# Kernel optimization log

Hardware: AMD Instinct MI355X
Metric: run time of the kernel (lower is better)

The kernel has to match this reference:

```python
import jax, jax.numpy as jnp
import numpy as np

NUM_LABELS = 80
GROUPS = 512
OUT_PER_GROUP = 4  # 2048 / 512
K = 14  # kernel == spatial size -> 1x1 output


def setup_inputs() -> dict:
    key = jax.random.key(0)
    ks = jax.random.split(key, 8)
    B = 256
    x = jax.random.normal(ks[0], (B, NUM_LABELS, K, K), dtype=jnp.float32)
    # conv1: 1x1, num_labels -> 512 (store as [out,in])
    w1 = jax.random.normal(ks[1], (512, NUM_LABELS), dtype=jnp.float32) * 0.05
    b1 = jax.random.normal(ks[2], (512,), dtype=jnp.float32) * 0.01
    # conv2: 1x1, 512 -> 512
    w2 = jax.random.normal(ks[3], (512, 512), dtype=jnp.float32) * 0.05
    b2 = jax.random.normal(ks[4], (512,), dtype=jnp.float32) * 0.01
    # conv3 (grouped): per group, 1 in-ch -> 4 out-ch, 14x14 kernel, no bias
    w3 = jax.random.normal(ks[5], (GROUPS, OUT_PER_GROUP, K, K), dtype=jnp.float32) * 0.02
    # fc: 2048 -> num_labels (torch Linear layout [out,in])
    fc_w = jax.random.normal(ks[6], (NUM_LABELS, GROUPS * OUT_PER_GROUP), dtype=jnp.float32) * 0.02
    fc_b = jax.random.normal(ks[7], (NUM_LABELS,), dtype=jnp.float32) * 0.01
    return {"x": x, "w1": w1, "b1": b1, "w2": w2, "b2": b2,
            "w3": w3, "fc_w": fc_w, "fc_b": fc_b}


def reference(x, w1, b1, w2, b2, w3, fc_w, fc_b):
    # conv1: 1x1 conv == channel GEMM. x: [B,C,H,W]
    h = jnp.einsum('bchw,oc->bohw', x, w1) + b1[None, :, None, None]
    # conv2: 1x1 conv, 512 -> 512
    h = jnp.einsum('bchw,oc->bohw', h, w2) + b2[None, :, None, None]
    # conv3: 512 independent group convs (1 in-ch each, full 14x14 kernel,
    # no padding) -> output spatial 1x1. Fused into a single contraction.
    # h: [B, G, H, W], w3: [G, O, H, W] -> [B, G, O]
    g = jnp.einsum('bghw,gohw->bgo', h, w3)
    g = jax.nn.relu(g)
    # torch.cat over groups then flatten == reshape [B, G*O]
    flat = g.reshape(g.shape[0], GROUPS * OUT_PER_GROUP)
    return flat @ fc_w.T + fc_b
```

## Files before the change

### kernel.cpp

```cpp
#include <hip/hip_runtime.h>
#include <hip/hip_bf16.h>

#define CIN 80
#define NSP 196
#define HWP 208
#define KP  96
#define XST 104

#define NBA 4096
#define NBB 1024
#define NBC 512
#define NBD 64
#define NBE 16

typedef __attribute__((ext_vector_type(8))) short  short8;
typedef __attribute__((ext_vector_type(4))) float  floatx4;
typedef __attribute__((ext_vector_type(4))) unsigned short ushort4v;

static __device__ __forceinline__ unsigned short f2b(float f) {
    __hip_bfloat16 h = __float2bfloat16(f);
    return *(unsigned short*)&h;
}
static __device__ __forceinline__ float b2f(unsigned short u) {
    unsigned int x = ((unsigned int)u) << 16;
    float f; __builtin_memcpy(&f, &x, 4); return f;
}

__global__ __launch_bounds__(384) void kPre(
    const float* __restrict__ x,  const float* __restrict__ w1,
    const float* __restrict__ b1, const float* __restrict__ w2,
    const float* __restrict__ b2, const float* __restrict__ w3,
    const float* __restrict__ fc_w, const float* __restrict__ fc_b,
    float* __restrict__ Wcf, unsigned short* __restrict__ xbf,
    unsigned short* __restrict__ w3tb, unsigned short* __restrict__ fctb,
    float* __restrict__ out)
{
    __shared__ float tile[80 * 53];
    const int blk = blockIdx.x, t = threadIdx.x;

    if (blk < NBA) {
        const int o4 = blk >> 5, kc = blk & 31;
        const int lc = t % 96, oi = t / 96;
        const int o = o4 * 4 + oi;
        const int m0 = kc * 16;
        if (lc <= CIN) {
            const float* __restrict__ w2p = w2 + (size_t)o * 512 + m0;
            float part = 0.f;
            if (lc < CIN) {
                const float* __restrict__ w1p = w1 + (size_t)m0 * CIN + lc;
                #pragma unroll
                for (int i = 0; i < 16; ++i)
                    part = fmaf(w2p[i], w1p[(size_t)i * CIN], part);
            } else {
                #pragma unroll
                for (int i = 0; i < 16; ++i)
                    part = fmaf(w2p[i], b1[m0 + i], part);
                if (kc == 31) part += b2[o];
            }
            atomicAdd(Wcf + o * KP + lc, part);
        }
    } else if (blk < NBA + NBB) {
        const int r = blk - NBA;
        const int b = r >> 2, qt = r & 3, hw0 = qt * 52;
        for (int idx = t; idx < 80 * 52; idx += 384) {
            const int k = idx / 52, hl = idx - k * 52;
            const int hw = hw0 + hl;
            tile[k * 53 + hl] = (hw < NSP) ? x[(size_t)b * CIN * NSP + k * NSP + hw] : 0.f;
        }
        __syncthreads();
        unsigned short* __restrict__ ob = xbf + (size_t)b * HWP * KP;
        for (int idx = t; idx < 52 * 24; idx += 384) {
            const int hl = idx / 24, kq = idx - hl * 24;
            const int hw = hw0 + hl;
            ushort4v v;
            #pragma unroll
            for (int j = 0; j < 4; ++j) {
                const int k = kq * 4 + j;
                float f = 0.f;
                if (hw < NSP) {
                    if (k < CIN) f = tile[k * 53 + hl];
                    else if (k == CIN) f = 1.f;
                }
                v[j] = f2b(f);
            }
            *(ushort4v*)(ob + (size_t)hw * KP + kq * 4) = v;
        }
    } else if (blk < NBA + NBB + NBC) {
        const int g = blk - NBA - NBB;
        if (t < HWP) {
            ushort4v v;
            #pragma unroll
            for (int o = 0; o < 4; ++o)
                v[o] = f2b((t < NSP) ? w3[(size_t)g * 4 * NSP + o * NSP + t] : 0.f);
            *(ushort4v*)(w3tb + ((size_t)g * HWP + t) * 4) = v;
        }
    } else if (blk < NBA + NBB + NBC + NBD) {
        const int base = (blk - NBA - NBB - NBC) * 2560;
        for (int i = t; i < 2560; i += 384) {
            const int idx = base + i;
            const int k = idx / CIN, l = idx - k * CIN;
            fctb[idx] = f2b(fc_w[(size_t)l * 2048 + k]);
        }
    } else {
        const int base = (blk - NBA - NBB - NBC - NBD) * 1280;
        for (int i = t; i < 1280; i += 384) {
            const int idx = base + i;
            out[idx] = fc_b[idx - (idx / CIN) * CIN];
        }
    }
}

__global__ __launch_bounds__(512) void kM(
    const unsigned short* __restrict__ xbf, const float* __restrict__ Wcf,
    const unsigned short* __restrict__ w3tb, const unsigned short* __restrict__ fctb,
    float* __restrict__ out)
{
    __shared__ __align__(16) unsigned short xs[HWP * XST];
    __shared__ float gl[1024];
    const int b = blockIdx.x, gc = blockIdx.y;
    const int t = threadIdx.x;

    {
        const ushort4v* __restrict__ src = (const ushort4v*)(xbf + (size_t)b * HWP * KP);
        for (int idx = t; idx < HWP * 24; idx += 512) {
            const int r = idx / 24, c = idx - r * 24;
            *(ushort4v*)(xs + r * XST + c * 4) = src[idx];
        }
    }

    const int w = t >> 6, lane = t & 63;
    const int col = lane & 15, quad = lane >> 4;
    const int gb = gc * 256 + w * 32;

    short8 A[2][3];
    #pragma unroll
    for (int mt = 0; mt < 2; ++mt) {
        const float* __restrict__ ap = Wcf + (size_t)(gb + mt * 16 + col) * KP + quad * 8;
        #pragma unroll
        for (int ks = 0; ks < 3; ++ks) {
            const floatx4 lo = *(const floatx4*)(ap + ks * 32);
            const floatx4 hi = *(const floatx4*)(ap + ks * 32 + 4);
            short8 s;
            #pragma unroll
            for (int j = 0; j < 4; ++j) {
                s[j]     = (short)f2b(lo[j]);
                s[4 + j] = (short)f2b(hi[j]);
            }
            A[mt][ks] = s;
        }
    }

    float p[2][4][4];
    #pragma unroll
    for (int mt = 0; mt < 2; ++mt)
        #pragma unroll
        for (int r = 0; r < 4; ++r)
            #pragma unroll
            for (int o = 0; o < 4; ++o) p[mt][r][o] = 0.f;

    const unsigned short* __restrict__ xrow = xs + col * XST + quad * 8;
    const unsigned short* __restrict__ wb0 =
        w3tb + ((size_t)(gb + quad * 4) * HWP + col) * 4;
    const unsigned short* __restrict__ wb1 =
        w3tb + ((size_t)(gb + 16 + quad * 4) * HWP + col) * 4;

    __syncthreads();

    #pragma unroll 1
    for (int nt = 0; nt < 13; ++nt) {
        ushort4v wv0[4], wv1[4];
        #pragma unroll
        for (int r = 0; r < 4; ++r) {
            wv0[r] = *(const ushort4v*)(wb0 + ((size_t)r * HWP + nt * 16) * 4);
            wv1[r] = *(const ushort4v*)(wb1 + ((size_t)r * HWP + nt * 16) * 4);
        }
        const unsigned short* __restrict__ xp = xrow + nt * 16 * XST;
        const short8 x0 = *(const short8*)(xp);
        const short8 x1 = *(const short8*)(xp + 32);
        const short8 x2 = *(const short8*)(xp + 64);
        floatx4 a0 = {0.f, 0.f, 0.f, 0.f}, a1 = {0.f, 0.f, 0.f, 0.f};
        a0 = __builtin_amdgcn_mfma_f32_16x16x32_bf16(A[0][0], x0, a0, 0, 0, 0);
        a0 = __builtin_amdgcn_mfma_f32_16x16x32_bf16(A[0][1], x1, a0, 0, 0, 0);
        a0 = __builtin_amdgcn_mfma_f32_16x16x32_bf16(A[0][2], x2, a0, 0, 0, 0);
        a1 = __builtin_amdgcn_mfma_f32_16x16x32_bf16(A[1][0], x0, a1, 0, 0, 0);
        a1 = __builtin_amdgcn_mfma_f32_16x16x32_bf16(A[1][1], x1, a1, 0, 0, 0);
        a1 = __builtin_amdgcn_mfma_f32_16x16x32_bf16(A[1][2], x2, a1, 0, 0, 0);
        #pragma unroll
        for (int r = 0; r < 4; ++r) {
            p[0][r][0] = fmaf(a0[r], b2f(wv0[r][0]), p[0][r][0]);
            p[0][r][1] = fmaf(a0[r], b2f(wv0[r][1]), p[0][r][1]);
            p[0][r][2] = fmaf(a0[r], b2f(wv0[r][2]), p[0][r][2]);
            p[0][r][3] = fmaf(a0[r], b2f(wv0[r][3]), p[0][r][3]);
            p[1][r][0] = fmaf(a1[r], b2f(wv1[r][0]), p[1][r][0]);
            p[1][r][1] = fmaf(a1[r], b2f(wv1[r][1]), p[1][r][1]);
            p[1][r][2] = fmaf(a1[r], b2f(wv1[r][2]), p[1][r][2]);
            p[1][r][3] = fmaf(a1[r], b2f(wv1[r][3]), p[1][r][3]);
        }
    }

    #pragma unroll
    for (int mt = 0; mt < 2; ++mt)
        #pragma unroll
        for (int r = 0; r < 4; ++r) {
            float q0 = p[mt][r][0], q1 = p[mt][r][1], q2 = p[mt][r][2], q3 = p[mt][r][3];
            #pragma unroll
            for (int s = 8; s >= 1; s >>= 1) {
                q0 += __shfl_down(q0, s, 16);
                q1 += __shfl_down(q1, s, 16);
                q2 += __shfl_down(q2, s, 16);
                q3 += __shfl_down(q3, s, 16);
            }
            if (col == 0) {
                const int glocal = w * 32 + mt * 16 + quad * 4 + r;
                floatx4 ov = {fmaxf(q0, 0.f), fmaxf(q1, 0.f), fmaxf(q2, 0.f), fmaxf(q3, 0.f)};
                *(floatx4*)(gl + glocal * 4) = ov;
            }
        }
    __syncthreads();

    if (t < 320) {
        const int l = t % CIN, q = t / CIN;
        const unsigned short* __restrict__ fr =
            fctb + (size_t)(gc * 1024 + q * 256) * CIN + l;
        const float* __restrict__ gp = gl + q * 256;
        float s = 0.f;
        #pragma unroll 4
        for (int kk = 0; kk < 256; ++kk)
            s = fmaf(gp[kk], b2f(fr[(size_t)kk * CIN]), s);
        atomicAdd(out + b * CIN + l, s);
    }
}

extern "C" void kernel_launch(void* const* d_in, const int* in_sizes, int n_in,
                              void* d_out, int out_size, void* d_ws, size_t ws_size,
                              hipStream_t stream) {
    const float* x    = (const float*)d_in[0];
    const float* w1   = (const float*)d_in[1];
    const float* b1   = (const float*)d_in[2];
    const float* w2   = (const float*)d_in[3];
    const float* b2   = (const float*)d_in[4];
    const float* w3   = (const float*)d_in[5];
    const float* fc_w = (const float*)d_in[6];
    const float* fc_b = (const float*)d_in[7];
    float* out = (float*)d_out;

    const int B = in_sizes[0] / (CIN * NSP);

    char* ws = (char*)d_ws;
    unsigned short* xbf = (unsigned short*)ws;
    size_t off = (size_t)B * HWP * KP * 2;
    float* Wcf = (float*)(ws + off);                   off += 512 * KP * 4;
    unsigned short* w3tb = (unsigned short*)(ws + off); off += (size_t)512 * HWP * 4 * 2;
    unsigned short* fctb = (unsigned short*)(ws + off);

    hipMemsetAsync(Wcf, 0, 512 * KP * 4, stream);
    kPre<<<NBA + NBB + NBC + NBD + NBE, 384, 0, stream>>>(
        x, w1, b1, w2, b2, w3, fc_w, fc_b, Wcf, xbf, w3tb, fctb, out);
    kM<<<dim3(B, 2), 512, 0, stream>>>(xbf, Wcf, w3tb, fctb, out);
}
```

Measured before the change: 138.3 us.

## Fuse x bf16 transpose into main kernel and replace atomics with split-K reduction

Removes the separate x transposition/bf16 staging pass by having the main kernel read fp32 x directly, convert it and transpose it into shared memory. The folded W2·W1 weight is now built as 8 partial slices plus a small reduction kernel that emits bf16, replacing the memset and float atomics. The main kernel now runs one 1024-thread block per batch covering all groups, and reduces the FC output in shared memory with the bias added, so the output atomics and the bias-init blocks are gone. The trade-offs are an extra kernel launch, strided transposing writes to shared memory, and half as many blocks in the main kernel.

```diff
diff --git a/kernel.cpp b/kernel.cpp
--- a/kernel.cpp
+++ b/kernel.cpp
@@ -7,11 +7,9 @@
 #define KP  96
 #define XST 104
 
-#define NBA 4096
-#define NBB 1024
+#define NBA 1024
 #define NBC 512
 #define NBD 64
-#define NBE 16
 
 typedef __attribute__((ext_vector_type(8))) short  short8;
 typedef __attribute__((ext_vector_type(4))) float  floatx4;
@@ -27,66 +25,35 @@
 }
 
 __global__ __launch_bounds__(384) void kPre(
-    const float* __restrict__ x,  const float* __restrict__ w1,
-    const float* __restrict__ b1, const float* __restrict__ w2,
-    const float* __restrict__ b2, const float* __restrict__ w3,
-    const float* __restrict__ fc_w, const float* __restrict__ fc_b,
-    float* __restrict__ Wcf, unsigned short* __restrict__ xbf,
-    unsigned short* __restrict__ w3tb, unsigned short* __restrict__ fctb,
-    float* __restrict__ out)
+    const float* __restrict__ w1, const float* __restrict__ b1,
+    const float* __restrict__ w2, const float* __restrict__ w3,
+    const float* __restrict__ fc_w,
+    float* __restrict__ Wcf8, unsigned short* __restrict__ w3tb,
+    unsigned short* __restrict__ fctb)
 {
-    __shared__ float tile[80 * 53];
     const int blk = blockIdx.x, t = threadIdx.x;
 
     if (blk < NBA) {
-        const int o4 = blk >> 5, kc = blk & 31;
-        const int lc = t % 96, oi = t / 96;
-        const int o = o4 * 4 + oi;
-        const int m0 = kc * 16;
-        if (lc <= CIN) {
+        const int o4 = blk >> 3, kc = blk & 7, m0 = kc * 64;
+        if (t < 324) {
+            const int lc = t % 81, oi = t / 81;
+            const int o = o4 * 4 + oi;
             const float* __restrict__ w2p = w2 + (size_t)o * 512 + m0;
             float part = 0.f;
             if (lc < CIN) {
                 const float* __restrict__ w1p = w1 + (size_t)m0 * CIN + lc;
-                #pragma unroll
-                for (int i = 0; i < 16; ++i)
+                #pragma unroll 8
+                for (int i = 0; i < 64; ++i)
                     part = fmaf(w2p[i], w1p[(size_t)i * CIN], part);
             } else {
-                #pragma unroll
-                for (int i = 0; i < 16; ++i)
+                #pragma unroll 8
+                for (int i = 0; i < 64; ++i)
                     part = fmaf(w2p[i], b1[m0 + i], part);
-                if (kc == 31) part += b2[o];
             }
-            atomicAdd(Wcf + o * KP + lc, part);
-        }
-    } else if (blk < NBA + NBB) {
-        const int r = blk - NBA;
-        const int b = r >> 2, qt = r & 3, hw0 = qt * 52;
-        for (int idx = t; idx < 80 * 52; idx += 384) {
-            const int k = idx / 52, hl = idx - k * 52;
-            const int hw = hw0 + hl;
-            tile[k * 53 + hl] = (hw < NSP) ? x[(size_t)b * CIN * NSP + k * NSP + hw] : 0.f;
-        }
-        __syncthreads();
-        unsigned short* __restrict__ ob = xbf + (size_t)b * HWP * KP;
-        for (int idx = t; idx < 52 * 24; idx += 384) {
-            const int hl = idx / 24, kq = idx - hl * 24;
-            const int hw = hw0 + hl;
-            ushort4v v;
-            #pragma unroll
-            for (int j = 0; j < 4; ++j) {
-                const int k = kq * 4 + j;
-                float f = 0.f;
-                if (hw < NSP) {
-                    if (k < CIN) f = tile[k * 53 + hl];
-                    else if (k == CIN) f = 1.f;
-                }
-                v[j] = f2b(f);
-            }
-            *(ushort4v*)(ob + (size_t)hw * KP + kq * 4) = v;
-        }
-    } else if (blk < NBA + NBB + NBC) {
-        const int g = blk - NBA - NBB;
+            Wcf8[((size_t)kc * 512 + o) * KP + lc] = part;
+        }
+    } else if (blk < NBA + NBC) {
+        const int g = blk - NBA;
         if (t < HWP) {
             ushort4v v;
             #pragma unroll
@@ -94,60 +61,68 @@
                 v[o] = f2b((t < NSP) ? w3[(size_t)g * 4 * NSP + o * NSP + t] : 0.f);
             *(ushort4v*)(w3tb + ((size_t)g * HWP + t) * 4) = v;
         }
-    } else if (blk < NBA + NBB + NBC + NBD) {
-        const int base = (blk - NBA - NBB - NBC) * 2560;
+    } else {
+        const int base = (blk - NBA - NBC) * 2560;
         for (int i = t; i < 2560; i += 384) {
             const int idx = base + i;
             const int k = idx / CIN, l = idx - k * CIN;
             fctb[idx] = f2b(fc_w[(size_t)l * 2048 + k]);
         }
-    } else {
-        const int base = (blk - NBA - NBB - NBC - NBD) * 1280;
-        for (int i = t; i < 1280; i += 384) {
-            const int idx = base + i;
-            out[idx] = fc_b[idx - (idx / CIN) * CIN];
-        }
-    }
-}
-
-__global__ __launch_bounds__(512) void kM(
-    const unsigned short* __restrict__ xbf, const float* __restrict__ Wcf,
+    }
+}
+
+__global__ __launch_bounds__(1024) void kRed(
+    const float* __restrict__ Wcf8, const float* __restrict__ b2,
+    unsigned short* __restrict__ Wcbf)
+{
+    const int idx = blockIdx.x * 1024 + threadIdx.x;
+    const int o = idx / KP, c = idx - o * KP;
+    float s = 0.f;
+    if (c <= CIN) {
+        #pragma unroll
+        for (int j = 0; j < 8; ++j)
+            s += Wcf8[((size_t)j * 512 + o) * KP + c];
+        if (c == CIN) s += b2[o];
+    }
+    Wcbf[idx] = f2b(s);
+}
+
+__global__ __launch_bounds__(1024) void kM(
+    const float* __restrict__ x, const unsigned short* __restrict__ Wcbf,
     const unsigned short* __restrict__ w3tb, const unsigned short* __restrict__ fctb,
-    float* __restrict__ out)
+    const float* __restrict__ fc_b, float* __restrict__ out)
 {
     __shared__ __align__(16) unsigned short xs[HWP * XST];
-    __shared__ float gl[1024];
-    const int b = blockIdx.x, gc = blockIdx.y;
-    const int t = threadIdx.x;
+    __shared__ float gl[2048];
+    const int b = blockIdx.x, t = threadIdx.x;
 
     {
-        const ushort4v* __restrict__ src = (const ushort4v*)(xbf + (size_t)b * HWP * KP);
-        for (int idx = t; idx < HWP * 24; idx += 512) {
-            const int r = idx / 24, c = idx - r * 24;
-            *(ushort4v*)(xs + r * XST + c * 4) = src[idx];
+        const float* __restrict__ xb = x + (size_t)b * CIN * NSP;
+        for (int idx = t; idx < CIN * NSP; idx += 1024) {
+            const int k = idx / NSP, hw = idx - k * NSP;
+            xs[hw * XST + k] = f2b(xb[idx]);
+        }
+        for (int idx = t; idx < NSP * 24; idx += 1024) {
+            const int hw = idx / 24, k = 80 + (idx - (idx / 24) * 24);
+            xs[hw * XST + k] = (k == CIN) ? (unsigned short)0x3F80 : (unsigned short)0;
+        }
+        for (int idx = t; idx < 12 * XST; idx += 1024) {
+            const int hw = NSP + idx / XST, k = idx - (idx / XST) * XST;
+            xs[hw * XST + k] = 0;
         }
     }
 
     const int w = t >> 6, lane = t & 63;
     const int col = lane & 15, quad = lane >> 4;
-    const int gb = gc * 256 + w * 32;
+    const int gb = w * 32;
 
     short8 A[2][3];
     #pragma unroll
     for (int mt = 0; mt < 2; ++mt) {
-        const float* __restrict__ ap = Wcf + (size_t)(gb + mt * 16 + col) * KP + quad * 8;
-        #pragma unroll
-        for (int ks = 0; ks < 3; ++ks) {
-            const floatx4 lo = *(const floatx4*)(ap + ks * 32);
-            const floatx4 hi = *(const floatx4*)(ap + ks * 32 + 4);
-            short8 s;
-            #pragma unroll
-            for (int j = 0; j < 4; ++j) {
-                s[j]     = (short)f2b(lo[j]);
-                s[4 + j] = (short)f2b(hi[j]);
-            }
-            A[mt][ks] = s;
-        }
+        const unsigned short* __restrict__ ap =
+            Wcbf + (size_t)(gb + mt * 16 + col) * KP + quad * 8;
+        #pragma unroll
+        for (int ks = 0; ks < 3; ++ks) A[mt][ks] = *(const short8*)(ap + ks * 32);
     }
 
     float p[2][4][4];
@@ -211,23 +186,30 @@
                 q3 += __shfl_down(q3, s, 16);
             }
             if (col == 0) {
-                const int glocal = w * 32 + mt * 16 + quad * 4 + r;
+                const int glocal = gb + mt * 16 + quad * 4 + r;
                 floatx4 ov = {fmaxf(q0, 0.f), fmaxf(q1, 0.f), fmaxf(q2, 0.f), fmaxf(q3, 0.f)};
                 *(floatx4*)(gl + glocal * 4) = ov;
             }
         }
     __syncthreads();
 
-    if (t < 320) {
-        const int l = t % CIN, q = t / CIN;
-        const unsigned short* __restrict__ fr =
-            fctb + (size_t)(gc * 1024 + q * 256) * CIN + l;
-        const float* __restrict__ gp = gl + q * 256;
+    float* pf = (float*)xs;
+    if (t < 640) {
+        const int l = t % CIN, part = t / CIN;
+        const unsigned short* __restrict__ fr = fctb + (size_t)(part * 256) * CIN + l;
+        const float* __restrict__ gp = gl + part * 256;
         float s = 0.f;
         #pragma unroll 4
         for (int kk = 0; kk < 256; ++kk)
             s = fmaf(gp[kk], b2f(fr[(size_t)kk * CIN]), s);
-        atomicAdd(out + b * CIN + l, s);
+        pf[t] = s;
+    }
+    __syncthreads();
+    if (t < CIN) {
+        float s = fc_b[t];
+        #pragma unroll
+        for (int j = 0; j < 8; ++j) s += pf[j * CIN + t];
+        out[b * CIN + t] = s;
     }
 }
 
@@ -247,14 +229,13 @@
     const int B = in_sizes[0] / (CIN * NSP);
 
     char* ws = (char*)d_ws;
-    unsigned short* xbf = (unsigned short*)ws;
-    size_t off = (size_t)B * HWP * KP * 2;
-    float* Wcf = (float*)(ws + off);                   off += 512 * KP * 4;
+    float* Wcf8 = (float*)ws;
+    size_t off = (size_t)8 * 512 * KP * 4;
+    unsigned short* Wcbf = (unsigned short*)(ws + off); off += 512 * KP * 2;
     unsigned short* w3tb = (unsigned short*)(ws + off); off += (size_t)512 * HWP * 4 * 2;
     unsigned short* fctb = (unsigned short*)(ws + off);
 
-    hipMemsetAsync(Wcf, 0, 512 * KP * 4, stream);
-    kPre<<<NBA + NBB + NBC + NBD + NBE, 384, 0, stream>>>(
-        x, w1, b1, w2, b2, w3, fc_w, fc_b, Wcf, xbf, w3tb, fctb, out);
-    kM<<<dim3(B, 2), 512, 0, stream>>>(xbf, Wcf, w3tb, fctb, out);
-}
+    kPre<<<NBA + NBC + NBD, 384, 0, stream>>>(w1, b1, w2, w3, fc_w, Wcf8, w3tb, fctb);
+    kRed<<<48, 1024, 0, stream>>>(Wcf8, b2, Wcbf);
+    kM<<<B, 1024, 0, stream>>>(x, Wcbf, w3tb, fctb, fc_b, out);
+}
```

After: 129.3 us. 6.5% less time.
